# Performance work log

Hardware: AMD Instinct MI355X
Metric: run time of the kernel (lower is better)

Reference implementation:

```python
import jax, jax.numpy as jnp
import numpy as np

NPOINT, RADIUS, NSAMPLE = 512, 0.2, 32
MLP = [64, 64, 128]
IN_CH = 67
EPS = 1e-5


def farthest_point_sample(xyz, npoint):
    # xyz: [B, N, 3] -> idx [B, npoint]. Deterministic start at index 0.
    B, N, _ = xyz.shape

    def step(carry, _):
        dist, far = carry  # dist [B,N], far [B]
        centroid = jnp.take_along_axis(xyz, far[:, None, None], axis=1)  # [B,1,3]
        d = jnp.sum((xyz - centroid) ** 2, axis=-1)  # [B,N]
        dist = jnp.minimum(dist, d)
        return (dist, jnp.argmax(dist, axis=-1).astype(jnp.int32)), far

    init = (jnp.full((B, N), 1e10, dtype=xyz.dtype), jnp.zeros((B,), jnp.int32))
    _, idxs = jax.lax.scan(step, init, None, length=npoint)
    return idxs.T  # [B, npoint]


def query_ball_point(radius, nsample, xyz, new_xyz):
    # xyz [B,N,3], new_xyz [B,S,3] -> idx [B,S,nsample]
    B, N, _ = xyz.shape
    sqr = jnp.sum((new_xyz[:, :, None, :] - xyz[:, None, :, :]) ** 2, axis=-1)  # [B,S,N]
    gidx = jnp.where(sqr > radius * radius, N, jnp.arange(N, dtype=jnp.int32))
    gidx = jnp.sort(gidx, axis=-1)[:, :, :nsample]
    first = gidx[:, :, :1]
    return jnp.where(gidx == N, first, gidx).astype(jnp.int32)


def gather_points(pts, idx):
    # pts [B,N,C], idx [B,...] -> [B,...,C]
    return jax.vmap(lambda p, i: p[i])(pts, idx)


def sample_and_group(npoint, radius, nsample, xyz, points):
    fps_idx = farthest_point_sample(xyz, npoint)          # [B,S]
    new_xyz = gather_points(xyz, fps_idx)                 # [B,S,3]
    idx = query_ball_point(radius, nsample, xyz, new_xyz)  # [B,S,K]
    grouped_xyz = gather_points(xyz, idx)                 # [B,S,K,3]
    grouped_xyz_norm = grouped_xyz - new_xyz[:, :, None, :]
    grouped_pts = gather_points(points, idx)              # [B,S,K,D]
    new_points = jnp.concatenate([grouped_xyz_norm, grouped_pts], axis=-1)  # [B,S,K,3+D]
    return new_xyz, new_points


def mlp_bn_relu(x, w, b, gamma, beta):
    # x [B,C,K,S]; 1x1 conv + training-mode BatchNorm2d + ReLU
    y = jnp.einsum('oc,bcks->boks', w, x) + b[None, :, None, None]
    mean = jnp.mean(y, axis=(0, 2, 3), keepdims=True)
    var = jnp.var(y, axis=(0, 2, 3), keepdims=True)
    y = (y - mean) * jax.lax.rsqrt(var + EPS)
    y = y * gamma[None, :, None, None] + beta[None, :, None, None]
    return jax.nn.relu(y)


def setup_inputs() -> dict:
    key = jax.random.key(0)
    ks = jax.random.split(key, 8)
    B, N, D = 16, 2048, 64
    inp = {
        'xyz': jax.random.normal(ks[0], (B, 3, N), jnp.float32),
        'points': jax.random.normal(ks[1], (B, D, N), jnp.float32),
    }
    last = IN_CH
    for i, out in enumerate(MLP):
        kw = jax.random.fold_in(ks[2], i)
        inp[f'w{i}'] = jax.random.normal(kw, (out, last), jnp.float32) * 0.05
        inp[f'b{i}'] = jnp.zeros((out,), jnp.float32)
        inp[f'g{i}'] = jnp.ones((out,), jnp.float32)
        inp[f'bt{i}'] = jnp.zeros((out,), jnp.float32)
        last = out
    return inp


def reference(xyz, points, w0, b0, g0, bt0, w1, b1, g1, bt1, w2, b2, g2, bt2):
    # xyz [B,3,N], points [B,D,N]
    xyz_t = jnp.transpose(xyz, (0, 2, 1))      # [B,N,3]
    pts_t = jnp.transpose(points, (0, 2, 1))   # [B,N,D]
    new_xyz, new_points = sample_and_group(NPOINT, RADIUS, NSAMPLE, xyz_t, pts_t)
    # [B,S,K,C] -> [B,C,K,S]
    x = jnp.transpose(new_points, (0, 3, 2, 1))
    for (w, b, g, bt) in ((w0, b0, g0, bt0), (w1, b1, g1, bt1), (w2, b2, g2, bt2)):
        x = mlp_bn_relu(x, w, b, g, bt)
    feature = jnp.max(x, axis=2)               # [B,C',S]
    new_xyz_out = jnp.transpose(new_xyz, (0, 2, 1))  # [B,3,S]
    return new_xyz_out, feature
```

## Files before the change

kernel.cpp:

```cpp
#include <hip/hip_runtime.h>
#include <hip/hip_bf16.h>
#include <stdint.h>

#define NB 16
#define NPT 2048
#define NS 512
#define NK 32
#define PTOT (NB*NS*NK)
#define C_IN 67
#define EPSV 1e-5f

typedef __attribute__((ext_vector_type(8))) short short8;
typedef __attribute__((ext_vector_type(4))) float floatx4;

#define WS_NEWXYZ 0
#define WS_GIDX   24576
#define WS_ST     286720
#define WS_W1BF   288256
#define WS_W2BF   290304
#define WS_RAWMAX 294400
#define WS_PTS_TB 818688
#define WS_Y1     1867264
#define WS_Y2     10255872
#define WS_Y3     18644480

__device__ __forceinline__ float bf2f(ushort u){ return __uint_as_float((uint32_t)u<<16); }
__device__ __forceinline__ ushort f2bf(float f){
  uint32_t u = __float_as_uint(f);
  return (ushort)((u + 0x7FFFu + ((u>>16)&1u)) >> 16);
}

template<int CTRL>
__device__ __forceinline__ double dppmax64f(double k){
  long long b = __double_as_longlong(k);
  int lo = (int)(uint32_t)b, hi = (int)(b>>32);
  int olo = __builtin_amdgcn_update_dpp(lo, lo, CTRL, 0xF, 0xF, false);
  int ohi = __builtin_amdgcn_update_dpp(hi, hi, CTRL, 0xF, 0xF, false);
  double o = __hiloint2double(ohi, olo);
  return fmax(o, k);
}
__device__ __forceinline__ unsigned long long u64max(unsigned long long a, unsigned long long b){ return a>b?a:b; }

__global__ __launch_bounds__(256) void prep_kernel(const float* __restrict__ xyz,
    float* __restrict__ nxyz, float* __restrict__ out0,
    const float* __restrict__ pts, ushort* __restrict__ pts_tb,
    const float* __restrict__ w1, const float* __restrict__ w2,
    ushort* __restrict__ w1b, ushort* __restrict__ w2b, float* __restrict__ st)
{
  __shared__ union {
    struct { float4 lc[NPT]; double warr[2][4]; int sel[NS]; } f;
    float tile[64][65];
  } sm;
  const int blk = blockIdx.x;
  const int tid = threadIdx.x;
  if (blk < 16){
    const int b = blk;
    const float* xb = xyz + (size_t)b*3*NPT;
    float px[8], py[8], pz[8], dist[8];
    uint32_t lo_[8];
    #pragma unroll
    for (int j=0;j<8;j++){
      int n = j*256 + tid;
      float x = xb[n], y = xb[NPT+n], z = xb[2*NPT+n];
      sm.f.lc[n] = make_float4(x,y,z,0.f);
      px[j]=x; py[j]=y; pz[j]=z; dist[j]=1e10f;
      lo_[j] = ~(uint32_t)n;
    }
    if (tid==0) sm.f.sel[0]=0;
    __syncthreads();
    float4 c0 = sm.f.lc[0];
    float cx = c0.x, cy = c0.y, cz = c0.z;
    const int lane = tid & 63, wid = tid >> 6;
    for (int t=1;t<NS;t++){
      double kk[8];
      #pragma unroll
      for (int j=0;j<8;j++){
        float dx = __fsub_rn(px[j], cx);
        float dy = __fsub_rn(py[j], cy);
        float dz = __fsub_rn(pz[j], cz);
        float d  = __fadd_rn(__fadd_rn(__fmul_rn(dx,dx),__fmul_rn(dy,dy)),__fmul_rn(dz,dz));
        float dd = fminf(dist[j], d);
        dist[j] = dd;
        kk[j] = __hiloint2double((int)__float_as_uint(dd), (int)lo_[j]);
      }
      double m0 = fmax(kk[0],kk[1]), m1 = fmax(kk[2],kk[3]);
      double m2 = fmax(kk[4],kk[5]), m3 = fmax(kk[6],kk[7]);
      double best = fmax(fmax(m0,m1), fmax(m2,m3));
      best = dppmax64f<0xB1>(best);
      best = dppmax64f<0x4E>(best);
      best = dppmax64f<0x124>(best);
      best = dppmax64f<0x128>(best);
      long long bb = __double_as_longlong(best);
      int bl = (int)(uint32_t)bb, bh = (int)(bb>>32);
      unsigned long long k0 = (((unsigned long long)(uint32_t)__builtin_amdgcn_readlane(bh, 0))<<32)  | (uint32_t)__builtin_amdgcn_readlane(bl, 0);
      unsigned long long k1 = (((unsigned long long)(uint32_t)__builtin_amdgcn_readlane(bh, 16))<<32) | (uint32_t)__builtin_amdgcn_readlane(bl, 16);
      unsigned long long k2 = (((unsigned long long)(uint32_t)__builtin_amdgcn_readlane(bh, 32))<<32) | (uint32_t)__builtin_amdgcn_readlane(bl, 32);
      unsigned long long k3 = (((unsigned long long)(uint32_t)__builtin_amdgcn_readlane(bh, 48))<<32) | (uint32_t)__builtin_amdgcn_readlane(bl, 48);
      unsigned long long kw = u64max(u64max(k0,k1), u64max(k2,k3));
      if (lane==0) sm.f.warr[t&1][wid] = __longlong_as_double((long long)kw);
      __syncthreads();
      double w0 = sm.f.warr[t&1][0], w1_ = sm.f.warr[t&1][1], w2_ = sm.f.warr[t&1][2], w3 = sm.f.warr[t&1][3];
      double f = fmax(fmax(w0,w1_), fmax(w2_,w3));
      int n = (int)(~(uint32_t)__double_as_longlong(f));
      float4 cc = sm.f.lc[n];
      cx = cc.x; cy = cc.y; cz = cc.z;
      if (tid==0) sm.f.sel[t]=n;
    }
    __syncthreads();
    for (int s = tid; s < NS; s += 256){
      int n = sm.f.sel[s];
      float4 cc = sm.f.lc[n];
      float* np_ = nxyz + ((size_t)b*NS + s)*3;
      np_[0]=cc.x; np_[1]=cc.y; np_[2]=cc.z;
      float* ob = out0 + (size_t)b*3*NS + s;
      ob[0]=cc.x; ob[NS]=cc.y; ob[2*NS]=cc.z;
    }
  } else if (blk < 528){
    const int t2 = blk - 16;
    const int b = t2 >> 5;
    const int n0 = (t2 & 31) * 64;
    const int lane = tid & 63;
    const int row4 = tid >> 6;
    const float* src = pts + (size_t)b*64*NPT;
    #pragma unroll
    for (int r=0; r<16; r++){
      int cc = r*4 + row4;
      sm.tile[cc][lane] = src[(size_t)cc*NPT + n0 + lane];
    }
    __syncthreads();
    ushort* dst = pts_tb + ((size_t)b*NPT + n0)*64;
    #pragma unroll
    for (int r=0; r<16; r++){
      int nn = r*4 + row4;
      dst[(size_t)nn*64 + lane] = f2bf(sm.tile[lane][nn]);
    }
  } else {
    for (int i = tid; i < 4096; i += 256) w1b[i] = f2bf(w1[i]);
    for (int i = tid; i < 8192; i += 256) w2b[i] = f2bf(w2[i]);
    for (int i = tid; i < 1536; i += 256) st[i] = 0.f;
  }
}

__global__ __launch_bounds__(256) void ballq_kernel(const float* __restrict__ xyz,
                                                    const float* __restrict__ nxyz,
                                                    int* __restrict__ gidx)
{
  const int g = blockIdx.x*4 + (threadIdx.x>>6);
  const int lane = threadIdx.x & 63;
  const int b = g >> 9;
  const float* xb = xyz + (size_t)b*3*NPT;
  const float* c = nxyz + (size_t)g*3;
  const float cx = c[0], cy = c[1], cz = c[2];
  const float r2 = 0.2f*0.2f;
  int cnt = 0; int first = 0;
  int* out = gidx + (size_t)g*NK;
  for (int ch=0; ch<NPT/64 && cnt<NK; ch++){
    int n = ch*64 + lane;
    float dx = __fsub_rn(cx, xb[n]);
    float dy = __fsub_rn(cy, xb[NPT+n]);
    float dz = __fsub_rn(cz, xb[2*NPT+n]);
    float d  = __fadd_rn(__fadd_rn(__fmul_rn(dx,dx),__fmul_rn(dy,dy)),__fmul_rn(dz,dz));
    bool in = (d <= r2);
    unsigned long long mask = __ballot(in);
    if (mask){
      if (cnt==0) first = ch*64 + (__ffsll((unsigned long long)mask)-1);
      if (in){
        int pos = cnt + __popcll(mask & ((1ull<<lane)-1ull));
        if (pos < NK) out[pos] = n;
      }
      cnt += __popcll(mask);
    }
  }
  if (cnt < NK && lane >= cnt && lane < NK) out[lane] = first;
}

__global__ __launch_bounds__(256) void conv1_kernel(const float* __restrict__ xyz,
    const ushort* __restrict__ pts_tb, const int* __restrict__ gidx,
    const float* __restrict__ nxyz, const float* __restrict__ Wt,
    const float* __restrict__ bias, ushort* __restrict__ y1)
{
  const int p = blockIdx.x*256 + threadIdx.x;
  const int bs = p >> 5;
  const int b = p >> 14;
  const int n = gidx[p];
  float x[C_IN];
  {
    const float* xb = xyz + (size_t)b*3*NPT;
    const float* cc = nxyz + (size_t)bs*3;
    x[0] = xb[n]        - cc[0];
    x[1] = xb[NPT+n]    - cc[1];
    x[2] = xb[2*NPT+n]  - cc[2];
    const ushort* pr = pts_tb + ((size_t)b*NPT + n)*64;
    #pragma unroll
    for (int q=0;q<8;q++){
      short8 v = *(const short8*)(pr + q*8);
      #pragma unroll
      for (int j=0;j<8;j++) x[3+8*q+j] = bf2f((ushort)v[j]);
    }
  }
  ushort* yr = y1 + (size_t)p*64;
  #pragma unroll 1
  for (int o=0;o<64;o+=8){
    float a[8];
    #pragma unroll
    for (int k=0;k<8;k++) a[k] = bias[o+k];
    #pragma unroll
    for (int c=0;c<C_IN;c++){
      float xv = x[c];
      #pragma unroll
      for (int k=0;k<8;k++) a[k] = fmaf(Wt[(o+k)*C_IN+c], xv, a[k]);
    }
    short8 sv;
    #pragma unroll
    for (int k=0;k<8;k++) sv[k] = (short)f2bf(a[k]);
    *(short8*)(yr + o) = sv;
  }
}

__global__ __launch_bounds__(256) void stats64_kernel(const ushort* __restrict__ y,
                                                      float* __restrict__ stbase)
{
  const int wid = threadIdx.x>>6, lane = threadIdx.x&63;
  const int oct = lane & 7, pr = lane >> 3;
  const int p0 = blockIdx.x*1024 + wid*256;
  float s[8], s2[8];
  #pragma unroll
  for (int j=0;j<8;j++){ s[j]=0.f; s2[j]=0.f; }
  for (int it=0; it<32; it++){
    int p = p0 + it*8 + pr;
    short8 v = *(const short8*)(y + (size_t)p*64 + oct*8);
    #pragma unroll
    for (int j=0;j<8;j++){
      float f = bf2f((ushort)v[j]);
      s[j] += f; s2[j] = fmaf(f,f,s2[j]);
    }
  }
  #pragma unroll
  for (int off=8; off<64; off<<=1){
    #pragma unroll
    for (int j=0;j<8;j++){ s[j] += __shfl_xor(s[j],off,64); s2[j] += __shfl_xor(s2[j],off,64); }
  }
  __shared__ float sd[4][128];
  if (pr==0){
    #pragma unroll
    for (int j=0;j<8;j++){ sd[wid][oct*8+j] = s[j]; sd[wid][64+oct*8+j] = s2[j]; }
  }
  __syncthreads();
  int t = threadIdx.x;
  if (t < 128){
    float v = sd[0][t]+sd[1][t]+sd[2][t]+sd[3][t];
    int rep = blockIdx.x & 1;
    float* dst = (t<64) ? (stbase + rep*64 + t) : (stbase + 128 + rep*64 + (t-64));
    atomicAdd(dst, v);
  }
}

__global__ __launch_bounds__(256) void conv2_mfma(const ushort* __restrict__ yin,
    const float* __restrict__ st, const float* __restrict__ g0, const float* __restrict__ bt0,
    const ushort* __restrict__ Wb, const float* __restrict__ bias,
    ushort* __restrict__ yout)
{
  __shared__ float aAl[64], aBl[64];
  const int tid = threadIdx.x;
  if (tid < 64){
    float s = st[tid] + st[64+tid];
    float qv = st[128+tid] + st[192+tid];
    float mean = s * (1.f/PTOT);
    float var  = qv * (1.f/PTOT) - mean*mean;
    float a = g0[tid] * rsqrtf(var + EPSV);
    aAl[tid] = a;
    aBl[tid] = fmaf(-mean, a, bt0[tid]);
  }
  __syncthreads();
  const int wid = tid>>6, lane = tid&63;
  const int q = lane>>4, nn = lane&15;
  const int p0 = (blockIdx.x*4 + wid) * 32;
  float a_[2][8], b_[2][8];
  #pragma unroll
  for (int kh=0;kh<2;kh++)
    #pragma unroll
    for (int j=0;j<8;j++){
      a_[kh][j] = aAl[kh*32 + q*8 + j];
      b_[kh][j] = aBl[kh*32 + q*8 + j];
    }
  short8 Af[4][2];
  #pragma unroll
  for (int mt=0;mt<4;mt++)
    #pragma unroll
    for (int kh=0;kh<2;kh++)
      Af[mt][kh] = *(const short8*)(Wb + (mt*16 + nn)*64 + kh*32 + q*8);
  float bias_[4][4];
  #pragma unroll
  for (int mt=0;mt<4;mt++)
    #pragma unroll
    for (int r=0;r<4;r++) bias_[mt][r] = bias[mt*16 + q*4 + r];
  floatx4 z = {0.f,0.f,0.f,0.f};
  floatx4 acc[4][2];
  #pragma unroll
  for (int mt=0;mt<4;mt++){ acc[mt][0]=z; acc[mt][1]=z; }
  #pragma unroll
  for (int nt=0;nt<2;nt++){
    #pragma unroll
    for (int kh=0;kh<2;kh++){
      short8 raw = *(const short8*)(yin + (size_t)(p0 + nt*16 + nn)*64 + kh*32 + q*8);
      short8 bf;
      #pragma unroll
      for (int j=0;j<8;j++){
        float f = bf2f((ushort)raw[j]);
        f = fmaxf(fmaf(f, a_[kh][j], b_[kh][j]), 0.f);
        bf[j] = (short)f2bf(f);
      }
      #pragma unroll
      for (int mt=0;mt<4;mt++)
        acc[mt][nt] = __builtin_amdgcn_mfma_f32_16x16x32_bf16(Af[mt][kh], bf, acc[mt][nt], 0,0,0);
    }
  }
  #pragma unroll
  for (int nt=0;nt<2;nt++){
    int p = p0 + nt*16 + nn;
    #pragma unroll
    for (int mt=0;mt<4;mt++){
      float v0 = acc[mt][nt][0] + bias_[mt][0];
      float v1 = acc[mt][nt][1] + bias_[mt][1];
      float v2 = acc[mt][nt][2] + bias_[mt][2];
      float v3 = acc[mt][nt][3] + bias_[mt][3];
      uint2 w;
      w.x = (uint32_t)f2bf(v0) | ((uint32_t)f2bf(v1)<<16);
      w.y = (uint32_t)f2bf(v2) | ((uint32_t)f2bf(v3)<<16);
      *(uint2*)(yout + (size_t)p*64 + mt*16 + q*4) = w;
    }
  }
}

__global__ __launch_bounds__(256) void conv3_mfma(const ushort* __restrict__ yin,
    const float* __restrict__ st, const float* __restrict__ g1, const float* __restrict__ bt1,
    const ushort* __restrict__ Wb, const float* __restrict__ bias,
    ushort* __restrict__ yout)
{
  __shared__ float aAl[64], aBl[64];
  const int tid = threadIdx.x;
  if (tid < 64){
    float s = st[256+tid] + st[320+tid];
    float qv = st[384+tid] + st[448+tid];
    float mean = s * (1.f/PTOT);
    float var  = qv * (1.f/PTOT) - mean*mean;
    float a = g1[tid] * rsqrtf(var + EPSV);
    aAl[tid] = a;
    aBl[tid] = fmaf(-mean, a, bt1[tid]);
  }
  __syncthreads();
  const int wid = tid>>6, lane = tid&63;
  const int q = lane>>4, nn = lane&15;
  const int p0 = (blockIdx.x*4 + wid) * 16;
  float a_[2][8], b_[2][8];
  #pragma unroll
  for (int kh=0;kh<2;kh++)
    #pragma unroll
    for (int j=0;j<8;j++){
      a_[kh][j] = aAl[kh*32 + q*8 + j];
      b_[kh][j] = aBl[kh*32 + q*8 + j];
    }
  short8 bfr[2];
  #pragma unroll
  for (int kh=0;kh<2;kh++){
    short8 raw = *(const short8*)(yin + (size_t)(p0 + nn)*64 + kh*32 + q*8);
    short8 bf;
    #pragma unroll
    for (int j=0;j<8;j++){
      float f = bf2f((ushort)raw[j]);
      f = fmaxf(fmaf(f, a_[kh][j], b_[kh][j]), 0.f);
      bf[j] = (short)f2bf(f);
    }
    bfr[kh] = bf;
  }
  #pragma unroll 1
  for (int mh=0;mh<2;mh++){
    floatx4 z = {0.f,0.f,0.f,0.f};
    floatx4 acc[4];
    short8 Af[4][2];
    #pragma unroll
    for (int mt=0;mt<4;mt++){
      acc[mt]=z;
      #pragma unroll
      for (int kh=0;kh<2;kh++)
        Af[mt][kh] = *(const short8*)(Wb + ((mh*4+mt)*16 + nn)*64 + kh*32 + q*8);
    }
    #pragma unroll
    for (int kh=0;kh<2;kh++)
      #pragma unroll
      for (int mt=0;mt<4;mt++)
        acc[mt] = __builtin_amdgcn_mfma_f32_16x16x32_bf16(Af[mt][kh], bfr[kh], acc[mt], 0,0,0);
    int p = p0 + nn;
    #pragma unroll
    for (int mt=0;mt<4;mt++){
      int m0 = (mh*4+mt)*16;
      float v0 = acc[mt][0] + bias[m0 + q*4 + 0];
      float v1 = acc[mt][1] + bias[m0 + q*4 + 1];
      float v2 = acc[mt][2] + bias[m0 + q*4 + 2];
      float v3 = acc[mt][3] + bias[m0 + q*4 + 3];
      uint2 w;
      w.x = (uint32_t)f2bf(v0) | ((uint32_t)f2bf(v1)<<16);
      w.y = (uint32_t)f2bf(v2) | ((uint32_t)f2bf(v3)<<16);
      *(uint2*)(yout + (size_t)p*128 + m0 + q*4) = w;
    }
  }
}

__global__ __launch_bounds__(256) void statsmax_kernel(const ushort* __restrict__ y,
    float* __restrict__ st, ushort* __restrict__ rawmax)
{
  const int wid = threadIdx.x>>6, lane = threadIdx.x&63;
  const int oct = lane & 15, pr = lane >> 4;
  const int g0 = (blockIdx.x*4 + wid) * 4;
  float s[8], s2[8];
  #pragma unroll
  for (int j=0;j<8;j++){ s[j]=0.f; s2[j]=0.f; }
  for (int gi=0; gi<4; gi++){
    int g = g0 + gi;
    float mx[8];
    #pragma unroll
    for (int j=0;j<8;j++) mx[j] = -1e30f;
    for (int it=0; it<8; it++){
      int p = g*32 + it*4 + pr;
      short8 v = *(const short8*)(y + (size_t)p*128 + oct*8);
      #pragma unroll
      for (int j=0;j<8;j++){
        float f = bf2f((ushort)v[j]);
        s[j] += f; s2[j] = fmaf(f,f,s2[j]);
        mx[j] = fmaxf(mx[j], f);
      }
    }
    #pragma unroll
    for (int j=0;j<8;j++){
      mx[j] = fmaxf(mx[j], __shfl_xor(mx[j],16,64));
      mx[j] = fmaxf(mx[j], __shfl_xor(mx[j],32,64));
    }
    if (pr==0){
      short8 sv;
      #pragma unroll
      for (int j=0;j<8;j++) sv[j] = (short)f2bf(mx[j]);
      *(short8*)(rawmax + (size_t)g*128 + oct*8) = sv;
    }
  }
  #pragma unroll
  for (int j=0;j<8;j++){
    s[j]  += __shfl_xor(s[j],16,64);  s[j]  += __shfl_xor(s[j],32,64);
    s2[j] += __shfl_xor(s2[j],16,64); s2[j] += __shfl_xor(s2[j],32,64);
  }
  __shared__ float sd[4][256];
  if (pr==0){
    #pragma unroll
    for (int j=0;j<8;j++){ sd[wid][oct*8+j] = s[j]; sd[wid][128+oct*8+j] = s2[j]; }
  }
  __syncthreads();
  int t = threadIdx.x;
  float v = sd[0][t]+sd[1][t]+sd[2][t]+sd[3][t];
  int rep = blockIdx.x & 3;
  float* dst = (t<128) ? (st + 512 + rep*128 + t) : (st + 1024 + rep*128 + (t-128));
  atomicAdd(dst, v);
}

__global__ __launch_bounds__(256) void finalize_kernel(const ushort* __restrict__ rawmax,
    const float* __restrict__ st, const float* __restrict__ g2, const float* __restrict__ bt2,
    float* __restrict__ out)
{
  __shared__ float tile[64][65];
  __shared__ float aAl[128], aBl[128];
  const int tid = threadIdx.x;
  if (tid < 128){
    float s = st[512+tid] + st[640+tid] + st[768+tid] + st[896+tid];
    float qv = st[1024+tid] + st[1152+tid] + st[1280+tid] + st[1408+tid];
    float mean = s * (1.f/PTOT);
    float var  = qv * (1.f/PTOT) - mean*mean;
    float a = g2[tid] * rsqrtf(var + EPSV);
    aAl[tid] = a;
    aBl[tid] = fmaf(-mean, a, bt2[tid]);
  }
  __syncthreads();
  const int b  = blockIdx.x >> 4;
  const int ct = (blockIdx.x >> 3) & 1;
  const int stt = blockIdx.x & 7;
  const int c0 = ct*64, s0 = stt*64;
  const int lane = tid & 63, wid = tid >> 6;
  #pragma unroll
  for (int r=0;r<16;r++){
    int sl = r*4 + wid;
    tile[sl][lane] = bf2f(rawmax[((size_t)(b*512 + s0 + sl))*128 + c0 + lane]);
  }
  __syncthreads();
  #pragma unroll
  for (int r=0;r<16;r++){
    int cl = r*4 + wid;
    float a = aAl[c0+cl], bb = aBl[c0+cl];
    out[((size_t)(b*128 + c0 + cl))*512 + s0 + lane] = fmaxf(fmaf(tile[lane][cl], a, bb), 0.f);
  }
}

extern "C" void kernel_launch(void* const* d_in, const int* in_sizes, int n_in,
                              void* d_out, int out_size, void* d_ws, size_t ws_size,
                              hipStream_t stream) {
  const float* xyz = (const float*)d_in[0];
  const float* pts = (const float*)d_in[1];
  const float* w0  = (const float*)d_in[2];
  const float* b0  = (const float*)d_in[3];
  const float* g0  = (const float*)d_in[4];
  const float* bt0 = (const float*)d_in[5];
  const float* w1  = (const float*)d_in[6];
  const float* b1  = (const float*)d_in[7];
  const float* g1  = (const float*)d_in[8];
  const float* bt1 = (const float*)d_in[9];
  const float* w2  = (const float*)d_in[10];
  const float* b2  = (const float*)d_in[11];
  const float* g2  = (const float*)d_in[12];
  const float* bt2 = (const float*)d_in[13];
  float* out = (float*)d_out;
  float* ws  = (float*)d_ws;

  float* nxyz   = ws + WS_NEWXYZ;
  int*   gidx   = (int*)(ws + WS_GIDX);
  float* st     = ws + WS_ST;
  ushort* w1b = (ushort*)(ws + WS_W1BF);
  ushort* w2b = (ushort*)(ws + WS_W2BF);
  ushort* rawmax = (ushort*)(ws + WS_RAWMAX);
  ushort* pts_tb = (ushort*)(ws + WS_PTS_TB);
  ushort* y1 = (ushort*)(ws + WS_Y1);
  ushort* y2 = (ushort*)(ws + WS_Y2);
  ushort* y3 = (ushort*)(ws + WS_Y3);

  prep_kernel<<<529,256,0,stream>>>(xyz, nxyz, out, pts, pts_tb, w1, w2, w1b, w2b, st);
  ballq_kernel<<<2048,256,0,stream>>>(xyz, nxyz, gidx);
  conv1_kernel<<<PTOT/256,256,0,stream>>>(xyz, pts_tb, gidx, nxyz, w0, b0, y1);
  stats64_kernel<<<256,256,0,stream>>>(y1, st);
  conv2_mfma<<<2048,256,0,stream>>>(y1, st, g0, bt0, w1b, b1, y2);
  stats64_kernel<<<256,256,0,stream>>>(y2, st + 256);
  conv3_mfma<<<4096,256,0,stream>>>(y2, st, g1, bt1, w2b, b2, y3);
  statsmax_kernel<<<512,256,0,stream>>>(y3, st, rawmax);
  finalize_kernel<<<256,256,0,stream>>>(rawmax, st, g2, bt2, out + NB*3*NS);
}
```

Before: 515.3 us.

## Fuse ball query and BN statistics into conv kernels, drop y3 buffer

Moves the ball query into conv1, which now keeps neighbour indices in shared memory instead of a global gidx array. BatchNorm sum and sum-of-squares are now computed inside the conv epilogues with DPP wavefront reductions and atomics spread over 32 replicas, so the separate stats kernels go away. conv3 stages its output tile in LDS and computes per-group max and statistics there, so the 128-channel y3 tensor is never written and read back. This cuts kernel launches and global memory traffic, at the cost of many more atomics and extra reduction work inside the conv kernels.

After: 604.0 us. +17.2%, slower.

```diff
diff --git a/kernel.cpp b/kernel.cpp
--- a/kernel.cpp
+++ b/kernel.cpp
@@ -14,15 +14,13 @@
 typedef __attribute__((ext_vector_type(4))) float floatx4;
 
 #define WS_NEWXYZ 0
-#define WS_GIDX   24576
-#define WS_ST     286720
-#define WS_W1BF   288256
-#define WS_W2BF   290304
-#define WS_RAWMAX 294400
-#define WS_PTS_TB 818688
-#define WS_Y1     1867264
-#define WS_Y2     10255872
-#define WS_Y3     18644480
+#define WS_ST     24576
+#define WS_W1BF   40960
+#define WS_W2BF   43008
+#define WS_RAWMAX 47104
+#define WS_PTS_TB 571392
+#define WS_Y1     1619968
+#define WS_Y2     10008576
 
 __device__ __forceinline__ float bf2f(ushort u){ return __uint_as_float((uint32_t)u<<16); }
 __device__ __forceinline__ ushort f2bf(float f){
@@ -40,6 +38,28 @@
   return fmax(o, k);
 }
 __device__ __forceinline__ unsigned long long u64max(unsigned long long a, unsigned long long b){ return a>b?a:b; }
+
+template<int CTRL>
+__device__ __forceinline__ float dppaddf(float v){
+  int o = __builtin_amdgcn_update_dpp(__float_as_int(v), __float_as_int(v), CTRL, 0xF, 0xF, false);
+  return v + __int_as_float(o);
+}
+__device__ __forceinline__ float wsum63(float v){
+  v = dppaddf<0xB1>(v);
+  v = dppaddf<0x4E>(v);
+  v = dppaddf<0x124>(v);
+  v = dppaddf<0x128>(v);
+  v = dppaddf<0x142>(v);
+  v = dppaddf<0x143>(v);
+  return v;
+}
+__device__ __forceinline__ float rowsum16(float v){
+  v = dppaddf<0xB1>(v);
+  v = dppaddf<0x4E>(v);
+  v = dppaddf<0x124>(v);
+  v = dppaddf<0x128>(v);
+  return v;
+}
 
 __global__ __launch_bounds__(256) void prep_kernel(const float* __restrict__ xyz,
     float* __restrict__ nxyz, float* __restrict__ out0,
@@ -137,55 +157,53 @@
   } else {
     for (int i = tid; i < 4096; i += 256) w1b[i] = f2bf(w1[i]);
     for (int i = tid; i < 8192; i += 256) w2b[i] = f2bf(w2[i]);
-    for (int i = tid; i < 1536; i += 256) st[i] = 0.f;
-  }
-}
-
-__global__ __launch_bounds__(256) void ballq_kernel(const float* __restrict__ xyz,
-                                                    const float* __restrict__ nxyz,
-                                                    int* __restrict__ gidx)
+    for (int i = tid; i < 16384; i += 256) st[i] = 0.f;
+  }
+}
+
+__global__ __launch_bounds__(256) void conv1_kernel(const float* __restrict__ xyz,
+    const ushort* __restrict__ pts_tb, const float* __restrict__ nxyz,
+    const float* __restrict__ Wt, const float* __restrict__ bias,
+    ushort* __restrict__ y1, float* __restrict__ st)
 {
-  const int g = blockIdx.x*4 + (threadIdx.x>>6);
-  const int lane = threadIdx.x & 63;
-  const int b = g >> 9;
+  __shared__ int gq[8][NK];
+  const int tid = threadIdx.x;
+  const int wid = tid>>6, lane = tid&63;
+  const int p0 = blockIdx.x*256;
+  const int bs0 = p0 >> 5;
+  const int b = p0 >> 14;
   const float* xb = xyz + (size_t)b*3*NPT;
-  const float* c = nxyz + (size_t)g*3;
-  const float cx = c[0], cy = c[1], cz = c[2];
   const float r2 = 0.2f*0.2f;
-  int cnt = 0; int first = 0;
-  int* out = gidx + (size_t)g*NK;
-  for (int ch=0; ch<NPT/64 && cnt<NK; ch++){
-    int n = ch*64 + lane;
-    float dx = __fsub_rn(cx, xb[n]);
-    float dy = __fsub_rn(cy, xb[NPT+n]);
-    float dz = __fsub_rn(cz, xb[2*NPT+n]);
-    float d  = __fadd_rn(__fadd_rn(__fmul_rn(dx,dx),__fmul_rn(dy,dy)),__fmul_rn(dz,dz));
-    bool in = (d <= r2);
-    unsigned long long mask = __ballot(in);
-    if (mask){
-      if (cnt==0) first = ch*64 + (__ffsll((unsigned long long)mask)-1);
-      if (in){
-        int pos = cnt + __popcll(mask & ((1ull<<lane)-1ull));
-        if (pos < NK) out[pos] = n;
+  for (int gi=0; gi<2; gi++){
+    const int gl = wid*2 + gi;
+    const float* c = nxyz + (size_t)(bs0+gl)*3;
+    const float cx = c[0], cy = c[1], cz = c[2];
+    int cnt = 0, first = 0;
+    for (int ch=0; ch<NPT/64 && cnt<NK; ch++){
+      int n = ch*64 + lane;
+      float dx = __fsub_rn(cx, xb[n]);
+      float dy = __fsub_rn(cy, xb[NPT+n]);
+      float dz = __fsub_rn(cz, xb[2*NPT+n]);
+      float d  = __fadd_rn(__fadd_rn(__fmul_rn(dx,dx),__fmul_rn(dy,dy)),__fmul_rn(dz,dz));
+      bool in = (d <= r2);
+      unsigned long long mask = __ballot(in);
+      if (mask){
+        if (cnt==0) first = ch*64 + (__ffsll((unsigned long long)mask)-1);
+        if (in){
+          int pos = cnt + __popcll(mask & ((1ull<<lane)-1ull));
+          if (pos < NK) gq[gl][pos] = n;
+        }
+        cnt += __popcll(mask);
       }
-      cnt += __popcll(mask);
-    }
-  }
-  if (cnt < NK && lane >= cnt && lane < NK) out[lane] = first;
-}
-
-__global__ __launch_bounds__(256) void conv1_kernel(const float* __restrict__ xyz,
-    const ushort* __restrict__ pts_tb, const int* __restrict__ gidx,
-    const float* __restrict__ nxyz, const float* __restrict__ Wt,
-    const float* __restrict__ bias, ushort* __restrict__ y1)
-{
-  const int p = blockIdx.x*256 + threadIdx.x;
+    }
+    if (cnt < NK && lane >= cnt && lane < NK) gq[gl][lane] = first;
+  }
+  __syncthreads();
+  const int p = p0 + tid;
   const int bs = p >> 5;
-  const int b = p >> 14;
-  const int n = gidx[p];
+  const int n = gq[tid>>5][tid&31];
   float x[C_IN];
   {
-    const float* xb = xyz + (size_t)b*3*NPT;
     const float* cc = nxyz + (size_t)bs*3;
     x[0] = xb[n]        - cc[0];
     x[1] = xb[NPT+n]    - cc[1];
@@ -198,6 +216,7 @@
       for (int j=0;j<8;j++) x[3+8*q+j] = bf2f((ushort)v[j]);
     }
   }
+  const int rep = (blockIdx.x*4 + wid) & 31;
   ushort* yr = y1 + (size_t)p*64;
   #pragma unroll 1
   for (int o=0;o<64;o+=8){
@@ -214,57 +233,29 @@
     #pragma unroll
     for (int k=0;k<8;k++) sv[k] = (short)f2bf(a[k]);
     *(short8*)(yr + o) = sv;
-  }
-}
-
-__global__ __launch_bounds__(256) void stats64_kernel(const ushort* __restrict__ y,
-                                                      float* __restrict__ stbase)
-{
-  const int wid = threadIdx.x>>6, lane = threadIdx.x&63;
-  const int oct = lane & 7, pr = lane >> 3;
-  const int p0 = blockIdx.x*1024 + wid*256;
-  float s[8], s2[8];
-  #pragma unroll
-  for (int j=0;j<8;j++){ s[j]=0.f; s2[j]=0.f; }
-  for (int it=0; it<32; it++){
-    int p = p0 + it*8 + pr;
-    short8 v = *(const short8*)(y + (size_t)p*64 + oct*8);
-    #pragma unroll
-    for (int j=0;j<8;j++){
-      float f = bf2f((ushort)v[j]);
-      s[j] += f; s2[j] = fmaf(f,f,s2[j]);
-    }
-  }
-  #pragma unroll
-  for (int off=8; off<64; off<<=1){
-    #pragma unroll
-    for (int j=0;j<8;j++){ s[j] += __shfl_xor(s[j],off,64); s2[j] += __shfl_xor(s2[j],off,64); }
-  }
-  __shared__ float sd[4][128];
-  if (pr==0){
-    #pragma unroll
-    for (int j=0;j<8;j++){ sd[wid][oct*8+j] = s[j]; sd[wid][64+oct*8+j] = s2[j]; }
-  }
-  __syncthreads();
-  int t = threadIdx.x;
-  if (t < 128){
-    float v = sd[0][t]+sd[1][t]+sd[2][t]+sd[3][t];
-    int rep = blockIdx.x & 1;
-    float* dst = (t<64) ? (stbase + rep*64 + t) : (stbase + 128 + rep*64 + (t-64));
-    atomicAdd(dst, v);
+    #pragma unroll
+    for (int k=0;k<8;k++){
+      float s  = wsum63(a[k]);
+      float q2 = wsum63(a[k]*a[k]);
+      if (lane==63){
+        atomicAdd(&st[rep*64 + o + k], s);
+        atomicAdd(&st[2048 + rep*64 + o + k], q2);
+      }
+    }
   }
 }
 
 __global__ __launch_bounds__(256) void conv2_mfma(const ushort* __restrict__ yin,
-    const float* __restrict__ st, const float* __restrict__ g0, const float* __restrict__ bt0,
+    float* __restrict__ st, const float* __restrict__ g0, const float* __restrict__ bt0,
     const ushort* __restrict__ Wb, const float* __restrict__ bias,
     ushort* __restrict__ yout)
 {
   __shared__ float aAl[64], aBl[64];
   const int tid = threadIdx.x;
   if (tid < 64){
-    float s = st[tid] + st[64+tid];
-    float qv = st[128+tid] + st[192+tid];
+    float s=0.f, qv=0.f;
+    #pragma unroll 4
+    for (int r=0;r<32;r++){ s += st[r*64 + tid]; qv += st[2048 + r*64 + tid]; }
     float mean = s * (1.f/PTOT);
     float var  = qv * (1.f/PTOT) - mean*mean;
     float a = g0[tid] * rsqrtf(var + EPSV);
@@ -275,6 +266,7 @@
   const int wid = tid>>6, lane = tid&63;
   const int q = lane>>4, nn = lane&15;
   const int p0 = (blockIdx.x*4 + wid) * 32;
+  const int rep = (blockIdx.x*4 + wid) & 31;
   float a_[2][8], b_[2][8];
   #pragma unroll
   for (int kh=0;kh<2;kh++)
@@ -316,32 +308,45 @@
     }
   }
   #pragma unroll
-  for (int nt=0;nt<2;nt++){
-    int p = p0 + nt*16 + nn;
-    #pragma unroll
-    for (int mt=0;mt<4;mt++){
-      float v0 = acc[mt][nt][0] + bias_[mt][0];
-      float v1 = acc[mt][nt][1] + bias_[mt][1];
-      float v2 = acc[mt][nt][2] + bias_[mt][2];
-      float v3 = acc[mt][nt][3] + bias_[mt][3];
+  for (int mt=0;mt<4;mt++){
+    float vv[2][4];
+    #pragma unroll
+    for (int nt=0;nt<2;nt++)
+      #pragma unroll
+      for (int r=0;r<4;r++) vv[nt][r] = acc[mt][nt][r] + bias_[mt][r];
+    #pragma unroll
+    for (int nt=0;nt<2;nt++){
+      int p = p0 + nt*16 + nn;
       uint2 w;
-      w.x = (uint32_t)f2bf(v0) | ((uint32_t)f2bf(v1)<<16);
-      w.y = (uint32_t)f2bf(v2) | ((uint32_t)f2bf(v3)<<16);
+      w.x = (uint32_t)f2bf(vv[nt][0]) | ((uint32_t)f2bf(vv[nt][1])<<16);
+      w.y = (uint32_t)f2bf(vv[nt][2]) | ((uint32_t)f2bf(vv[nt][3])<<16);
       *(uint2*)(yout + (size_t)p*64 + mt*16 + q*4) = w;
     }
+    #pragma unroll
+    for (int r=0;r<4;r++){
+      float s  = rowsum16(vv[0][r] + vv[1][r]);
+      float q2 = rowsum16(vv[0][r]*vv[0][r] + vv[1][r]*vv[1][r]);
+      if (nn==0){
+        int ch = mt*16 + q*4 + r;
+        atomicAdd(&st[4096 + rep*64 + ch], s);
+        atomicAdd(&st[6144 + rep*64 + ch], q2);
+      }
+    }
   }
 }
 
 __global__ __launch_bounds__(256) void conv3_mfma(const ushort* __restrict__ yin,
-    const float* __restrict__ st, const float* __restrict__ g1, const float* __restrict__ bt1,
+    float* __restrict__ st, const float* __restrict__ g1, const float* __restrict__ bt1,
     const ushort* __restrict__ Wb, const float* __restrict__ bias,
-    ushort* __restrict__ yout)
+    ushort* __restrict__ rawmax)
 {
+  __shared__ ushort tile[64*132];
   __shared__ float aAl[64], aBl[64];
   const int tid = threadIdx.x;
   if (tid < 64){
-    float s = st[256+tid] + st[320+tid];
-    float qv = st[384+tid] + st[448+tid];
+    float s=0.f, qv=0.f;
+    #pragma unroll 4
+    for (int r=0;r<32;r++){ s += st[4096 + r*64 + tid]; qv += st[6144 + r*64 + tid]; }
     float mean = s * (1.f/PTOT);
     float var  = qv * (1.f/PTOT) - mean*mean;
     float a = g1[tid] * rsqrtf(var + EPSV);
@@ -390,7 +395,6 @@
       #pragma unroll
       for (int mt=0;mt<4;mt++)
         acc[mt] = __builtin_amdgcn_mfma_f32_16x16x32_bf16(Af[mt][kh], bfr[kh], acc[mt], 0,0,0);
-    int p = p0 + nn;
     #pragma unroll
     for (int mt=0;mt<4;mt++){
       int m0 = (mh*4+mt)*16;
@@ -401,63 +405,25 @@
       uint2 w;
       w.x = (uint32_t)f2bf(v0) | ((uint32_t)f2bf(v1)<<16);
       w.y = (uint32_t)f2bf(v2) | ((uint32_t)f2bf(v3)<<16);
-      *(uint2*)(yout + (size_t)p*128 + m0 + q*4) = w;
-    }
-  }
-}
-
-__global__ __launch_bounds__(256) void statsmax_kernel(const ushort* __restrict__ y,
-    float* __restrict__ st, ushort* __restrict__ rawmax)
-{
-  const int wid = threadIdx.x>>6, lane = threadIdx.x&63;
-  const int oct = lane & 15, pr = lane >> 4;
-  const int g0 = (blockIdx.x*4 + wid) * 4;
-  float s[8], s2[8];
-  #pragma unroll
-  for (int j=0;j<8;j++){ s[j]=0.f; s2[j]=0.f; }
-  for (int gi=0; gi<4; gi++){
-    int g = g0 + gi;
-    float mx[8];
-    #pragma unroll
-    for (int j=0;j<8;j++) mx[j] = -1e30f;
-    for (int it=0; it<8; it++){
-      int p = g*32 + it*4 + pr;
-      short8 v = *(const short8*)(y + (size_t)p*128 + oct*8);
-      #pragma unroll
-      for (int j=0;j<8;j++){
-        float f = bf2f((ushort)v[j]);
-        s[j] += f; s2[j] = fmaf(f,f,s2[j]);
-        mx[j] = fmaxf(mx[j], f);
-      }
-    }
-    #pragma unroll
-    for (int j=0;j<8;j++){
-      mx[j] = fmaxf(mx[j], __shfl_xor(mx[j],16,64));
-      mx[j] = fmaxf(mx[j], __shfl_xor(mx[j],32,64));
-    }
-    if (pr==0){
-      short8 sv;
-      #pragma unroll
-      for (int j=0;j<8;j++) sv[j] = (short)f2bf(mx[j]);
-      *(short8*)(rawmax + (size_t)g*128 + oct*8) = sv;
-    }
-  }
-  #pragma unroll
-  for (int j=0;j<8;j++){
-    s[j]  += __shfl_xor(s[j],16,64);  s[j]  += __shfl_xor(s[j],32,64);
-    s2[j] += __shfl_xor(s2[j],16,64); s2[j] += __shfl_xor(s2[j],32,64);
-  }
-  __shared__ float sd[4][256];
-  if (pr==0){
-    #pragma unroll
-    for (int j=0;j<8;j++){ sd[wid][oct*8+j] = s[j]; sd[wid][128+oct*8+j] = s2[j]; }
+      *(uint2*)&tile[(wid*16 + nn)*132 + m0 + q*4] = w;
+    }
   }
   __syncthreads();
-  int t = threadIdx.x;
-  float v = sd[0][t]+sd[1][t]+sd[2][t]+sd[3][t];
-  int rep = blockIdx.x & 3;
-  float* dst = (t<128) ? (st + 512 + rep*128 + t) : (st + 1024 + rep*128 + (t-128));
-  atomicAdd(dst, v);
+  const int c = tid >> 1, half = tid & 1;
+  float s = 0.f, q2 = 0.f, mx = -1e30f;
+  #pragma unroll 4
+  for (int it=0; it<32; it++){
+    float f = bf2f(tile[(half*32 + it)*132 + c]);
+    s += f; q2 = fmaf(f,f,q2); mx = fmaxf(mx, f);
+  }
+  rawmax[(size_t)(blockIdx.x*2 + half)*128 + c] = f2bf(mx);
+  s  += __shfl_xor(s, 1, 64);
+  q2 += __shfl_xor(q2, 1, 64);
+  if (half==0){
+    int rep = blockIdx.x & 31;
+    atomicAdd(&st[8192  + rep*128 + c], s);
+    atomicAdd(&st[12288 + rep*128 + c], q2);
+  }
 }
 
 __global__ __launch_bounds__(256) void finalize_kernel(const ushort* __restrict__ rawmax,
@@ -468,8 +434,9 @@
   __shared__ float aAl[128], aBl[128];
   const int tid = threadIdx.x;
   if (tid < 128){
-    float s = st[512+tid] + st[640+tid] + st[768+tid] + st[896+tid];
-    float qv = st[1024+tid] + st[1152+tid] + st[1280+tid] + st[1408+tid];
+    float s=0.f, qv=0.f;
+    #pragma unroll 4
+    for (int r=0;r<32;r++){ s += st[8192 + r*128 + tid]; qv += st[12288 + r*128 + tid]; }
     float mean = s * (1.f/PTOT);
     float var  = qv * (1.f/PTOT) - mean*mean;
     float a = g2[tid] * rsqrtf(var + EPSV);
@@ -516,24 +483,18 @@
   float* out = (float*)d_out;
   float* ws  = (float*)d_ws;
 
-  float* nxyz   = ws + WS_NEWXYZ;
-  int*   gidx   = (int*)(ws + WS_GIDX);
-  float* st     = ws + WS_ST;
+  float* nxyz = ws + WS_NEWXYZ;
+  float* st   = ws + WS_ST;
   ushort* w1b = (ushort*)(ws + WS_W1BF);
   ushort* w2b = (ushort*)(ws + WS_W2BF);
   ushort* rawmax = (ushort*)(ws + WS_RAWMAX);
   ushort* pts_tb = (ushort*)(ws + WS_PTS_TB);
   ushort* y1 = (ushort*)(ws + WS_Y1);
   ushort* y2 = (ushort*)(ws + WS_Y2);
-  ushort* y3 = (ushort*)(ws + WS_Y3);
 
   prep_kernel<<<529,256,0,stream>>>(xyz, nxyz, out, pts, pts_tb, w1, w2, w1b, w2b, st);
-  ballq_kernel<<<2048,256,0,stream>>>(xyz, nxyz, gidx);
-  conv1_kernel<<<PTOT/256,256,0,stream>>>(xyz, pts_tb, gidx, nxyz, w0, b0, y1);
-  stats64_kernel<<<256,256,0,stream>>>(y1, st);
+  conv1_kernel<<<PTOT/256,256,0,stream>>>(xyz, pts_tb, nxyz, w0, b0, y1, st);
   conv2_mfma<<<2048,256,0,stream>>>(y1, st, g0, bt0, w1b, b1, y2);
-  stats64_kernel<<<256,256,0,stream>>>(y2, st + 256);
-  conv3_mfma<<<4096,256,0,stream>>>(y2, st, g1, bt1, w2b, b2, y3);
-  statsmax_kernel<<<512,256,0,stream>>>(y3, st, rawmax);
+  conv3_mfma<<<4096,256,0,stream>>>(y2, st, g1, bt1, w2b, b2, rawmax);
   finalize_kernel<<<256,256,0,stream>>>(rawmax, st, g2, bt2, out + NB*3*NS);
 }
```
